# Optimization experiments

Measured on AMD Instinct MI355X. Metric: run time of the kernel, lower is better.

Reference implementation:

```python
import jax, jax.numpy as jnp
import numpy as np

B, IN, HID, OUT = 65536, 128, 256, 8


def setup_inputs() -> dict:
    key = jax.random.key(0)
    ks = jax.random.split(key, 9)
    def lin(kw, fan_in, fan_out):
        # torch nn.Linear default init: U(-1/sqrt(fan_in), 1/sqrt(fan_in))
        bound = 1.0 / np.sqrt(fan_in)
        kw1, kw2 = jax.random.split(kw)
        W = jax.random.uniform(kw1, (fan_out, fan_in), jnp.float32, -bound, bound)
        b = jax.random.uniform(kw2, (fan_out,), jnp.float32, -bound, bound)
        return W, b
    W1, b1 = lin(ks[0], 2 * IN, HID)
    W2, b2 = lin(ks[1], 2 * IN, HID)
    W3, b3 = lin(ks[2], HID + 3 * IN, HID)
    W4, b4 = lin(ks[3], HID, OUT)
    state = jax.random.normal(ks[4], (B, 3, IN), jnp.float32)
    return {"state": state, "W1": W1, "b1": b1, "W2": W2, "b2": b2,
            "W3": W3, "b3": b3, "W4": W4, "b4": b4}


def reference(state, W1, b1, W2, b2, W3, b3, W4, b4):
    # local_inputs = first 3 agents (state already [B,3,IN])
    local = state[:, :3]                              # [B,3,IN]
    agent = jnp.broadcast_to(local[:, :1], (local.shape[0], 2, local.shape[2]))
    neighbors = local[:, 1:3]                          # [B,2,IN]
    agents = jnp.concatenate([agent, neighbors], axis=-1)  # [B,2,2*IN]
    h_ij = jax.nn.relu(jnp.einsum('bnd,hd->bnh', agents, W1) + b1)  # [B,2,HID]
    e_ij = jax.nn.relu(jnp.einsum('bnd,hd->bnh', agents, W2) + b2)  # [B,2,HID]
    a_ij = jax.nn.softmax(e_ij, axis=1)                # softmax over neighbor dim
    h_i = jnp.sum(a_ij * h_ij, axis=1)                 # [B,HID]
    xxx = jnp.concatenate([h_i, local.reshape(local.shape[0], -1)], axis=-1)
    xxx = jax.nn.relu(xxx @ W3.T + b3)                 # [B,HID]
    return jnp.tanh(xxx @ W4.T + b4)                   # [B,OUT]
```

## Files before the change

### kernel.cpp

```cpp
#include <hip/hip_runtime.h>

typedef __bf16 bf16x8 __attribute__((ext_vector_type(8)));
typedef float  f32x4  __attribute__((ext_vector_type(4)));

__device__ __forceinline__ unsigned short f2bf(float f) {
  unsigned int u = __builtin_bit_cast(unsigned int, f);
  u = u + 0x7fffu + ((u >> 16) & 1u);
  return (unsigned short)(u >> 16);
}

#define O_W2 65536
#define O_W3 131072
#define O_W4 294912
#define N_PREP 299008

__global__ void prep_kernel(const float* __restrict__ W1, const float* __restrict__ W2,
                            const float* __restrict__ W3, const float* __restrict__ W4,
                            unsigned short* __restrict__ ws) {
  int id = blockIdx.x * 256 + threadIdx.x;
  if (id < O_W2) {
    ws[id] = f2bf(W1[id]);
  } else if (id < O_W3) {
    ws[id] = f2bf(W2[id - O_W2]);
  } else if (id < O_W4) {
    ws[id] = f2bf(W3[id - O_W3]);
  } else if (id < N_PREP) {
    int t = id - O_W4;
    ws[id] = (t < 2048) ? f2bf(W4[t]) : (unsigned short)0;
  }
}

#define XSTR 648
#define YSTR 264

__global__ __launch_bounds__(512, 2) void actor_kernel(
    const float* __restrict__ state,
    const float* __restrict__ b1, const float* __restrict__ b2,
    const float* __restrict__ b3, const float* __restrict__ b4,
    const unsigned short* __restrict__ wsb,
    float* __restrict__ out)
{
  __shared__ unsigned short xxx[64 * XSTR];
  __shared__ unsigned short ytl[64 * YSTR];

  const int tid  = threadIdx.x;
  const int w    = tid >> 6;
  const int lane = tid & 63;
  const int lr   = lane & 15;
  const int lg   = lane >> 4;
  const long b0  = (long)blockIdx.x * 64;

  {
    const float4* sp = (const float4*)(state + b0 * 384);
    #pragma unroll
    for (int t = 0; t < 12; ++t) {
      int f = tid + t * 512;
      float4 v = sp[f];
      int r   = f / 96;
      int rem = f - r * 96;
      int i   = rem >> 5;
      int k4  = (rem & 31) << 2;
      ushort4 u;
      u.x = f2bf(v.x); u.y = f2bf(v.y); u.z = f2bf(v.z); u.w = f2bf(v.w);
      *(ushort4*)&xxx[r * XSTR + 256 + i * 128 + k4] = u;
    }
  }
  __syncthreads();

  const int n0 = w * 32;

  #pragma unroll
  for (int sc = 0; sc < 2; ++sc) {
    const int ncol = n0 + sc * 16 + lr;
    f32x4 accH[8], accE[8];
    #pragma unroll
    for (int rt = 0; rt < 8; ++rt) {
      accH[rt] = (f32x4){0.f, 0.f, 0.f, 0.f};
      accE[rt] = (f32x4){0.f, 0.f, 0.f, 0.f};
    }
    const unsigned short* w1p = wsb + ncol * 256 + lg * 8;
    const unsigned short* w2p = wsb + O_W2 + ncol * 256 + lg * 8;

    bf16x8 bh = *(const bf16x8*)(w1p);
    bf16x8 be = *(const bf16x8*)(w2p);
    #pragma unroll
    for (int ks = 0; ks < 8; ++ks) {
      bf16x8 bhn, ben;
      if (ks < 7) {
        bhn = *(const bf16x8*)(w1p + (ks + 1) * 32);
        ben = *(const bf16x8*)(w2p + (ks + 1) * 32);
      }
      const int colo = (ks < 4) ? (256 + ks * 32 + lg * 8)
                                : (384 + (ks - 4) * 32 + lg * 8);
      #pragma unroll
      for (int rt = 0; rt < 8; ++rt) {
        const int m = rt * 16 + lr;
        const int addr = (m >> 1) * XSTR + colo + ((ks >= 4) ? ((m & 1) << 7) : 0);
        bf16x8 a = *(const bf16x8*)&xxx[addr];
        accH[rt] = __builtin_amdgcn_mfma_f32_16x16x32_bf16(a, bh, accH[rt], 0, 0, 0);
        accE[rt] = __builtin_amdgcn_mfma_f32_16x16x32_bf16(a, be, accE[rt], 0, 0, 0);
      }
      bh = bhn; be = ben;
    }

    const float b1v = b1[ncol];
    const float b2v = b2[ncol];
    #pragma unroll
    for (int rt = 0; rt < 8; ++rt) {
      const int r0 = rt * 8 + lg * 2;
      #pragma unroll
      for (int pr = 0; pr < 2; ++pr) {
        float h0 = fmaxf(accH[rt][2 * pr + 0] + b1v, 0.f);
        float h1 = fmaxf(accH[rt][2 * pr + 1] + b1v, 0.f);
        float e0 = fmaxf(accE[rt][2 * pr + 0] + b2v, 0.f);
        float e1 = fmaxf(accE[rt][2 * pr + 1] + b2v, 0.f);
        float a0 = 1.0f / (1.0f + __expf(e1 - e0));
        float hi = h1 + a0 * (h0 - h1);
        xxx[(r0 + pr) * XSTR + ncol] = f2bf(hi);
      }
    }
  }
  __syncthreads();

  {
    f32x4 acc3[4][2];
    #pragma unroll
    for (int rt = 0; rt < 4; ++rt) {
      acc3[rt][0] = (f32x4){0.f, 0.f, 0.f, 0.f};
      acc3[rt][1] = (f32x4){0.f, 0.f, 0.f, 0.f};
    }
    const unsigned short* w3pa = wsb + O_W3 + (n0 + lr) * 640 + lg * 8;
    const unsigned short* w3pb = wsb + O_W3 + (n0 + 16 + lr) * 640 + lg * 8;
    bf16x8 ba = *(const bf16x8*)(w3pa);
    bf16x8 bb = *(const bf16x8*)(w3pb);
    for (int ks = 0; ks < 20; ++ks) {
      bf16x8 ban, bbn;
      if (ks < 19) {
        ban = *(const bf16x8*)(w3pa + (ks + 1) * 32);
        bbn = *(const bf16x8*)(w3pb + (ks + 1) * 32);
      }
      #pragma unroll
      for (int rt = 0; rt < 4; ++rt) {
        bf16x8 a = *(const bf16x8*)&xxx[(rt * 16 + lr) * XSTR + ks * 32 + lg * 8];
        acc3[rt][0] = __builtin_amdgcn_mfma_f32_16x16x32_bf16(a, ba, acc3[rt][0], 0, 0, 0);
        acc3[rt][1] = __builtin_amdgcn_mfma_f32_16x16x32_bf16(a, bb, acc3[rt][1], 0, 0, 0);
      }
      ba = ban; bb = bbn;
    }
    const float b3a = b3[n0 + lr];
    const float b3b = b3[n0 + 16 + lr];
    #pragma unroll
    for (int rt = 0; rt < 4; ++rt) {
      #pragma unroll
      for (int reg = 0; reg < 4; ++reg) {
        int row = rt * 16 + lg * 4 + reg;
        float va = fmaxf(acc3[rt][0][reg] + b3a, 0.f);
        float vb = fmaxf(acc3[rt][1][reg] + b3b, 0.f);
        ytl[row * YSTR + n0 + lr]      = f2bf(va);
        ytl[row * YSTR + n0 + 16 + lr] = f2bf(vb);
      }
    }
  }
  __syncthreads();

  if (w < 4) {
    f32x4 acc4 = (f32x4){0.f, 0.f, 0.f, 0.f};
    const unsigned short* w4p = wsb + O_W4 + lr * 256 + lg * 8;
    #pragma unroll
    for (int ks = 0; ks < 8; ++ks) {
      bf16x8 a = *(const bf16x8*)&ytl[(w * 16 + lr) * YSTR + ks * 32 + lg * 8];
      bf16x8 b = *(const bf16x8*)(w4p + ks * 32);
      acc4 = __builtin_amdgcn_mfma_f32_16x16x32_bf16(a, b, acc4, 0, 0, 0);
    }
    if (lr < 8) {
      const float b4v = b4[lr];
      #pragma unroll
      for (int reg = 0; reg < 4; ++reg) {
        long row = b0 + w * 16 + lg * 4 + reg;
        out[row * 8 + lr] = tanhf(acc4[reg] + b4v);
      }
    }
  }
}

extern "C" void kernel_launch(void* const* d_in, const int* in_sizes, int n_in,
                              void* d_out, int out_size, void* d_ws, size_t ws_size,
                              hipStream_t stream) {
  const float* state = (const float*)d_in[0];
  const float* W1 = (const float*)d_in[1];
  const float* b1 = (const float*)d_in[2];
  const float* W2 = (const float*)d_in[3];
  const float* b2 = (const float*)d_in[4];
  const float* W3 = (const float*)d_in[5];
  const float* b3 = (const float*)d_in[6];
  const float* W4 = (const float*)d_in[7];
  const float* b4 = (const float*)d_in[8];

  unsigned short* wsb = (unsigned short*)d_ws;

  prep_kernel<<<(N_PREP + 255) / 256, 256, 0, stream>>>(W1, W2, W3, W4, wsb);
  actor_kernel<<<1024, 512, 0, stream>>>(state, b1, b2, b3, b4, wsb, (float*)d_out);
}
```

Measured before the change: 241.6 us.

## Retile MFMA warps 2D, XOR-swizzle shared memory, reuse one LDS buffer, raise occupancy

Replaces the padded shared-memory strides with an XOR swizzle on a 640-wide row and drops the separate ytl buffer, writing the layer-3 output back into xxx after an extra barrier. This shrinks LDS use so launch bounds can ask for four blocks per CU. Warps are retiled in 2D for layers 1 and 3 so each A fragment feeds four MFMAs, which cuts LDS reads per MFMA. tanhf is also replaced with an exp-based formula. In exchange the kernel carries more accumulators, which raises register pressure against the higher occupancy target.

```diff
diff --git a/kernel.cpp b/kernel.cpp
--- a/kernel.cpp
+++ b/kernel.cpp
@@ -30,18 +30,18 @@
   }
 }
 
-#define XSTR 648
-#define YSTR 264
-
-__global__ __launch_bounds__(512, 2) void actor_kernel(
+#define SX(r, c) ((r) * 640 + ((c) ^ (((r) & 7) << 3)))
+
+#define MFMA __builtin_amdgcn_mfma_f32_16x16x32_bf16
+
+__global__ __launch_bounds__(512, 4) void actor_kernel(
     const float* __restrict__ state,
     const float* __restrict__ b1, const float* __restrict__ b2,
     const float* __restrict__ b3, const float* __restrict__ b4,
     const unsigned short* __restrict__ wsb,
     float* __restrict__ out)
 {
-  __shared__ unsigned short xxx[64 * XSTR];
-  __shared__ unsigned short ytl[64 * YSTR];
+  __shared__ __align__(16) unsigned short xxx[64 * 640];
 
   const int tid  = threadIdx.x;
   const int w    = tid >> 6;
@@ -62,103 +62,131 @@
       int k4  = (rem & 31) << 2;
       ushort4 u;
       u.x = f2bf(v.x); u.y = f2bf(v.y); u.z = f2bf(v.z); u.w = f2bf(v.w);
-      *(ushort4*)&xxx[r * XSTR + 256 + i * 128 + k4] = u;
-    }
-  }
-  __syncthreads();
-
-  const int n0 = w * 32;
-
+      *(ushort4*)&xxx[SX(r, 256 + i * 128 + k4)] = u;
+    }
+  }
+  __syncthreads();
+
+  const int wm = w >> 2;
+  const int wn = w & 3;
   #pragma unroll
   for (int sc = 0; sc < 2; ++sc) {
-    const int ncol = n0 + sc * 16 + lr;
-    f32x4 accH[8], accE[8];
-    #pragma unroll
-    for (int rt = 0; rt < 8; ++rt) {
-      accH[rt] = (f32x4){0.f, 0.f, 0.f, 0.f};
-      accE[rt] = (f32x4){0.f, 0.f, 0.f, 0.f};
-    }
-    const unsigned short* w1p = wsb + ncol * 256 + lg * 8;
-    const unsigned short* w2p = wsb + O_W2 + ncol * 256 + lg * 8;
-
-    bf16x8 bh = *(const bf16x8*)(w1p);
-    bf16x8 be = *(const bf16x8*)(w2p);
+    const int nb = wn * 64 + sc * 32;
+    f32x4 acc[4][4];
+    #pragma unroll
+    for (int rt = 0; rt < 4; ++rt)
+      #pragma unroll
+      for (int c = 0; c < 4; ++c)
+        acc[rt][c] = (f32x4){0.f, 0.f, 0.f, 0.f};
+
+    const unsigned short* w1p = wsb + (nb + lr) * 256 + lg * 8;
+    const unsigned short* w2p = wsb + O_W2 + (nb + lr) * 256 + lg * 8;
+    bf16x8 bh0 = *(const bf16x8*)(w1p);
+    bf16x8 bh1 = *(const bf16x8*)(w1p + 16 * 256);
+    bf16x8 be0 = *(const bf16x8*)(w2p);
+    bf16x8 be1 = *(const bf16x8*)(w2p + 16 * 256);
+    const float bv1a = b1[nb + lr], bv1b = b1[nb + 16 + lr];
+    const float bv2a = b2[nb + lr], bv2b = b2[nb + 16 + lr];
+
     #pragma unroll
     for (int ks = 0; ks < 8; ++ks) {
-      bf16x8 bhn, ben;
+      bf16x8 nh0, nh1, ne0, ne1;
       if (ks < 7) {
-        bhn = *(const bf16x8*)(w1p + (ks + 1) * 32);
-        ben = *(const bf16x8*)(w2p + (ks + 1) * 32);
+        nh0 = *(const bf16x8*)(w1p + (ks + 1) * 32);
+        nh1 = *(const bf16x8*)(w1p + 16 * 256 + (ks + 1) * 32);
+        ne0 = *(const bf16x8*)(w2p + (ks + 1) * 32);
+        ne1 = *(const bf16x8*)(w2p + 16 * 256 + (ks + 1) * 32);
       }
       const int colo = (ks < 4) ? (256 + ks * 32 + lg * 8)
                                 : (384 + (ks - 4) * 32 + lg * 8);
-      #pragma unroll
-      for (int rt = 0; rt < 8; ++rt) {
-        const int m = rt * 16 + lr;
-        const int addr = (m >> 1) * XSTR + colo + ((ks >= 4) ? ((m & 1) << 7) : 0);
-        bf16x8 a = *(const bf16x8*)&xxx[addr];
-        accH[rt] = __builtin_amdgcn_mfma_f32_16x16x32_bf16(a, bh, accH[rt], 0, 0, 0);
-        accE[rt] = __builtin_amdgcn_mfma_f32_16x16x32_bf16(a, be, accE[rt], 0, 0, 0);
-      }
-      bh = bhn; be = ben;
-    }
-
-    const float b1v = b1[ncol];
-    const float b2v = b2[ncol];
-    #pragma unroll
-    for (int rt = 0; rt < 8; ++rt) {
-      const int r0 = rt * 8 + lg * 2;
+      const int po   = (ks >= 4) ? ((lr & 1) << 7) : 0;
+      #pragma unroll
+      for (int rt = 0; rt < 4; ++rt) {
+        const int r = wm * 32 + rt * 8 + (lr >> 1);
+        bf16x8 a = *(const bf16x8*)&xxx[SX(r, colo + po)];
+        acc[rt][0] = MFMA(a, bh0, acc[rt][0], 0, 0, 0);
+        acc[rt][1] = MFMA(a, bh1, acc[rt][1], 0, 0, 0);
+        acc[rt][2] = MFMA(a, be0, acc[rt][2], 0, 0, 0);
+        acc[rt][3] = MFMA(a, be1, acc[rt][3], 0, 0, 0);
+      }
+      if (ks < 7) { bh0 = nh0; bh1 = nh1; be0 = ne0; be1 = ne1; }
+    }
+
+    #pragma unroll
+    for (int rt = 0; rt < 4; ++rt) {
       #pragma unroll
       for (int pr = 0; pr < 2; ++pr) {
-        float h0 = fmaxf(accH[rt][2 * pr + 0] + b1v, 0.f);
-        float h1 = fmaxf(accH[rt][2 * pr + 1] + b1v, 0.f);
-        float e0 = fmaxf(accE[rt][2 * pr + 0] + b2v, 0.f);
-        float e1 = fmaxf(accE[rt][2 * pr + 1] + b2v, 0.f);
-        float a0 = 1.0f / (1.0f + __expf(e1 - e0));
-        float hi = h1 + a0 * (h0 - h1);
-        xxx[(r0 + pr) * XSTR + ncol] = f2bf(hi);
-      }
-    }
-  }
-  __syncthreads();
+        const int r = wm * 32 + rt * 8 + lg * 2 + pr;
+        {
+          float h0 = fmaxf(acc[rt][0][2 * pr + 0] + bv1a, 0.f);
+          float h1 = fmaxf(acc[rt][0][2 * pr + 1] + bv1a, 0.f);
+          float e0 = fmaxf(acc[rt][2][2 * pr + 0] + bv2a, 0.f);
+          float e1 = fmaxf(acc[rt][2][2 * pr + 1] + bv2a, 0.f);
+          float a0 = 1.0f / (1.0f + __expf(e1 - e0));
+          xxx[SX(r, nb + lr)] = f2bf(h1 + a0 * (h0 - h1));
+        }
+        {
+          float h0 = fmaxf(acc[rt][1][2 * pr + 0] + bv1b, 0.f);
+          float h1 = fmaxf(acc[rt][1][2 * pr + 1] + bv1b, 0.f);
+          float e0 = fmaxf(acc[rt][3][2 * pr + 0] + bv2b, 0.f);
+          float e1 = fmaxf(acc[rt][3][2 * pr + 1] + bv2b, 0.f);
+          float a0 = 1.0f / (1.0f + __expf(e1 - e0));
+          xxx[SX(r, nb + 16 + lr)] = f2bf(h1 + a0 * (h0 - h1));
+        }
+      }
+    }
+  }
+  __syncthreads();
+
+  const int wm3 = w & 1;
+  const int wn3 = w >> 1;
+  f32x4 acc3[2][4];
+  #pragma unroll
+  for (int rt = 0; rt < 2; ++rt)
+    #pragma unroll
+    for (int nt = 0; nt < 4; ++nt)
+      acc3[rt][nt] = (f32x4){0.f, 0.f, 0.f, 0.f};
 
   {
-    f32x4 acc3[4][2];
-    #pragma unroll
-    for (int rt = 0; rt < 4; ++rt) {
-      acc3[rt][0] = (f32x4){0.f, 0.f, 0.f, 0.f};
-      acc3[rt][1] = (f32x4){0.f, 0.f, 0.f, 0.f};
-    }
-    const unsigned short* w3pa = wsb + O_W3 + (n0 + lr) * 640 + lg * 8;
-    const unsigned short* w3pb = wsb + O_W3 + (n0 + 16 + lr) * 640 + lg * 8;
-    bf16x8 ba = *(const bf16x8*)(w3pa);
-    bf16x8 bb = *(const bf16x8*)(w3pb);
+    const unsigned short* w3p = wsb + O_W3 + (wn3 * 64 + lr) * 640 + lg * 8;
+    bf16x8 c0 = *(const bf16x8*)(w3p);
+    bf16x8 c1 = *(const bf16x8*)(w3p + 16 * 640);
+    bf16x8 c2 = *(const bf16x8*)(w3p + 32 * 640);
+    bf16x8 c3 = *(const bf16x8*)(w3p + 48 * 640);
     for (int ks = 0; ks < 20; ++ks) {
-      bf16x8 ban, bbn;
+      bf16x8 d0, d1, d2, d3;
       if (ks < 19) {
-        ban = *(const bf16x8*)(w3pa + (ks + 1) * 32);
-        bbn = *(const bf16x8*)(w3pb + (ks + 1) * 32);
-      }
-      #pragma unroll
-      for (int rt = 0; rt < 4; ++rt) {
-        bf16x8 a = *(const bf16x8*)&xxx[(rt * 16 + lr) * XSTR + ks * 32 + lg * 8];
-        acc3[rt][0] = __builtin_amdgcn_mfma_f32_16x16x32_bf16(a, ba, acc3[rt][0], 0, 0, 0);
-        acc3[rt][1] = __builtin_amdgcn_mfma_f32_16x16x32_bf16(a, bb, acc3[rt][1], 0, 0, 0);
-      }
-      ba = ban; bb = bbn;
-    }
-    const float b3a = b3[n0 + lr];
-    const float b3b = b3[n0 + 16 + lr];
-    #pragma unroll
-    for (int rt = 0; rt < 4; ++rt) {
-      #pragma unroll
-      for (int reg = 0; reg < 4; ++reg) {
-        int row = rt * 16 + lg * 4 + reg;
-        float va = fmaxf(acc3[rt][0][reg] + b3a, 0.f);
-        float vb = fmaxf(acc3[rt][1][reg] + b3b, 0.f);
-        ytl[row * YSTR + n0 + lr]      = f2bf(va);
-        ytl[row * YSTR + n0 + 16 + lr] = f2bf(vb);
-      }
+        d0 = *(const bf16x8*)(w3p + (ks + 1) * 32);
+        d1 = *(const bf16x8*)(w3p + 16 * 640 + (ks + 1) * 32);
+        d2 = *(const bf16x8*)(w3p + 32 * 640 + (ks + 1) * 32);
+        d3 = *(const bf16x8*)(w3p + 48 * 640 + (ks + 1) * 32);
+      }
+      #pragma unroll
+      for (int rt = 0; rt < 2; ++rt) {
+        bf16x8 a = *(const bf16x8*)&xxx[SX(wm3 * 32 + rt * 16 + lr, ks * 32 + lg * 8)];
+        acc3[rt][0] = MFMA(a, c0, acc3[rt][0], 0, 0, 0);
+        acc3[rt][1] = MFMA(a, c1, acc3[rt][1], 0, 0, 0);
+        acc3[rt][2] = MFMA(a, c2, acc3[rt][2], 0, 0, 0);
+        acc3[rt][3] = MFMA(a, c3, acc3[rt][3], 0, 0, 0);
+      }
+      if (ks < 19) { c0 = d0; c1 = d1; c2 = d2; c3 = d3; }
+    }
+  }
+  const float bv3_0 = b3[wn3 * 64 + lr];
+  const float bv3_1 = b3[wn3 * 64 + 16 + lr];
+  const float bv3_2 = b3[wn3 * 64 + 32 + lr];
+  const float bv3_3 = b3[wn3 * 64 + 48 + lr];
+  __syncthreads();
+
+  #pragma unroll
+  for (int rt = 0; rt < 2; ++rt) {
+    #pragma unroll
+    for (int reg = 0; reg < 4; ++reg) {
+      const int row = wm3 * 32 + rt * 16 + lg * 4 + reg;
+      xxx[SX(row, wn3 * 64 + lr)]      = f2bf(fmaxf(acc3[rt][0][reg] + bv3_0, 0.f));
+      xxx[SX(row, wn3 * 64 + 16 + lr)] = f2bf(fmaxf(acc3[rt][1][reg] + bv3_1, 0.f));
+      xxx[SX(row, wn3 * 64 + 32 + lr)] = f2bf(fmaxf(acc3[rt][2][reg] + bv3_2, 0.f));
+      xxx[SX(row, wn3 * 64 + 48 + lr)] = f2bf(fmaxf(acc3[rt][3][reg] + bv3_3, 0.f));
     }
   }
   __syncthreads();
@@ -168,16 +196,19 @@
     const unsigned short* w4p = wsb + O_W4 + lr * 256 + lg * 8;
     #pragma unroll
     for (int ks = 0; ks < 8; ++ks) {
-      bf16x8 a = *(const bf16x8*)&ytl[(w * 16 + lr) * YSTR + ks * 32 + lg * 8];
+      bf16x8 a = *(const bf16x8*)&xxx[SX(w * 16 + lr, ks * 32 + lg * 8)];
       bf16x8 b = *(const bf16x8*)(w4p + ks * 32);
-      acc4 = __builtin_amdgcn_mfma_f32_16x16x32_bf16(a, b, acc4, 0, 0, 0);
+      acc4 = MFMA(a, b, acc4, 0, 0, 0);
     }
     if (lr < 8) {
       const float b4v = b4[lr];
       #pragma unroll
       for (int reg = 0; reg < 4; ++reg) {
+        float x = acc4[reg] + b4v;
+        float z = __expf(-2.f * fabsf(x));
+        float t = (1.f - z) / (1.f + z);
         long row = b0 + w * 16 + lg * 4 + reg;
-        out[row * 8 + lr] = tanhf(acc4[reg] + b4v);
+        out[row * 8 + lr] = copysignf(t, x);
       }
     }
   }
```

Result: slower. 286.6 us (+18.6%).

## Swizzle shared tile, merge H/E GEMMs into one MFMA, reuse LDS buffer

Applied to the files above, without the earlier changes.

Replaces padded LDS strides with an XOR-swizzled 640-wide layout and drops the separate ytl buffer, reusing xxx for the layer-3 output after an extra barrier. The first stage now packs W1 and W2 columns into one 16-wide MFMA tile (8 H + 8 E columns) and exchanges E values via shfl_xor, which halves the accumulator count. Weight loads use a 3-deep register ring prefetch, and tanhf is replaced by an exp-based formula. Occupancy hint goes from 2 to 4 blocks per CU, trading fewer registers and less LDS per block for more waves in flight. The cost is an extra barrier and more loop iterations in stage one.

```diff
diff --git a/kernel.cpp b/kernel.cpp
--- a/kernel.cpp
+++ b/kernel.cpp
@@ -30,18 +30,17 @@
   }
 }
 
-#define XSTR 648
-#define YSTR 264
-
-__global__ __launch_bounds__(512, 2) void actor_kernel(
+#define SX(r, c) ((r) * 640 + ((c) ^ (((r) & 7) << 3)))
+#define MFMA __builtin_amdgcn_mfma_f32_16x16x32_bf16
+
+__global__ __launch_bounds__(512, 4) void actor_kernel(
     const float* __restrict__ state,
     const float* __restrict__ b1, const float* __restrict__ b2,
     const float* __restrict__ b3, const float* __restrict__ b4,
     const unsigned short* __restrict__ wsb,
     float* __restrict__ out)
 {
-  __shared__ unsigned short xxx[64 * XSTR];
-  __shared__ unsigned short ytl[64 * YSTR];
+  __shared__ __align__(16) unsigned short xxx[64 * 640];
 
   const int tid  = threadIdx.x;
   const int w    = tid >> 6;
@@ -53,111 +52,110 @@
   {
     const float4* sp = (const float4*)(state + b0 * 384);
     #pragma unroll
-    for (int t = 0; t < 12; ++t) {
-      int f = tid + t * 512;
+    for (int i = 0; i < 12; ++i) {
+      int f = tid + i * 512;
       float4 v = sp[f];
-      int r   = f / 96;
-      int rem = f - r * 96;
-      int i   = rem >> 5;
-      int k4  = (rem & 31) << 2;
+      int r = f / 96, rem = f - r * 96;
       ushort4 u;
       u.x = f2bf(v.x); u.y = f2bf(v.y); u.z = f2bf(v.z); u.w = f2bf(v.w);
-      *(ushort4*)&xxx[r * XSTR + 256 + i * 128 + k4] = u;
+      *(ushort4*)&xxx[SX(r, 256 + rem * 4)] = u;
     }
   }
   __syncthreads();
 
-  const int n0 = w * 32;
-
-  #pragma unroll
-  for (int sc = 0; sc < 2; ++sc) {
-    const int ncol = n0 + sc * 16 + lr;
-    f32x4 accH[8], accE[8];
+  #pragma unroll 1
+  for (int p = 0; p < 4; ++p) {
+    const int cb = w * 32 + p * 8;
+    const unsigned short* wp = (lr < 8)
+        ? (wsb + (cb + lr) * 256 + lg * 8)
+        : (wsb + O_W2 + (cb + (lr - 8)) * 256 + lg * 8);
+    const float bv1 = b1[cb + (lr & 7)];
+    const float bv2 = b2[cb + (lr & 7)];
+
+    bf16x8 ring[4];
+    ring[0] = *(const bf16x8*)(wp);
+    ring[1] = *(const bf16x8*)(wp + 32);
+    ring[2] = *(const bf16x8*)(wp + 64);
+
+    f32x4 acc[8];
+    #pragma unroll
+    for (int rt = 0; rt < 8; ++rt) acc[rt] = (f32x4){0.f, 0.f, 0.f, 0.f};
+
+    #pragma unroll
+    for (int ks = 0; ks < 8; ++ks) {
+      if (ks < 5) ring[(ks + 3) & 3] = *(const bf16x8*)(wp + (ks + 3) * 32);
+      const int colk = (ks < 4) ? (256 + ks * 32 + lg * 8)
+                                : (384 + ((lr & 1) << 7) + (ks - 4) * 32 + lg * 8);
+      #pragma unroll
+      for (int rt = 0; rt < 8; ++rt) {
+        const int r = rt * 8 + (lr >> 1);
+        bf16x8 a = *(const bf16x8*)&xxx[SX(r, colk)];
+        acc[rt] = MFMA(a, ring[ks & 3], acc[rt], 0, 0, 0);
+      }
+    }
+
     #pragma unroll
     for (int rt = 0; rt < 8; ++rt) {
-      accH[rt] = (f32x4){0.f, 0.f, 0.f, 0.f};
-      accE[rt] = (f32x4){0.f, 0.f, 0.f, 0.f};
-    }
-    const unsigned short* w1p = wsb + ncol * 256 + lg * 8;
-    const unsigned short* w2p = wsb + O_W2 + ncol * 256 + lg * 8;
-
-    bf16x8 bh = *(const bf16x8*)(w1p);
-    bf16x8 be = *(const bf16x8*)(w2p);
-    #pragma unroll
-    for (int ks = 0; ks < 8; ++ks) {
-      bf16x8 bhn, ben;
-      if (ks < 7) {
-        bhn = *(const bf16x8*)(w1p + (ks + 1) * 32);
-        ben = *(const bf16x8*)(w2p + (ks + 1) * 32);
-      }
-      const int colo = (ks < 4) ? (256 + ks * 32 + lg * 8)
-                                : (384 + (ks - 4) * 32 + lg * 8);
-      #pragma unroll
-      for (int rt = 0; rt < 8; ++rt) {
-        const int m = rt * 16 + lr;
-        const int addr = (m >> 1) * XSTR + colo + ((ks >= 4) ? ((m & 1) << 7) : 0);
-        bf16x8 a = *(const bf16x8*)&xxx[addr];
-        accH[rt] = __builtin_amdgcn_mfma_f32_16x16x32_bf16(a, bh, accH[rt], 0, 0, 0);
-        accE[rt] = __builtin_amdgcn_mfma_f32_16x16x32_bf16(a, be, accE[rt], 0, 0, 0);
-      }
-      bh = bhn; be = ben;
-    }
-
-    const float b1v = b1[ncol];
-    const float b2v = b2[ncol];
-    #pragma unroll
-    for (int rt = 0; rt < 8; ++rt) {
-      const int r0 = rt * 8 + lg * 2;
-      #pragma unroll
-      for (int pr = 0; pr < 2; ++pr) {
-        float h0 = fmaxf(accH[rt][2 * pr + 0] + b1v, 0.f);
-        float h1 = fmaxf(accH[rt][2 * pr + 1] + b1v, 0.f);
-        float e0 = fmaxf(accE[rt][2 * pr + 0] + b2v, 0.f);
-        float e1 = fmaxf(accE[rt][2 * pr + 1] + b2v, 0.f);
-        float a0 = 1.0f / (1.0f + __expf(e1 - e0));
-        float hi = h1 + a0 * (h0 - h1);
-        xxx[(r0 + pr) * XSTR + ncol] = f2bf(hi);
+      float o0 = __shfl_xor(acc[rt][0], 8);
+      float o1 = __shfl_xor(acc[rt][1], 8);
+      float o2 = __shfl_xor(acc[rt][2], 8);
+      float o3 = __shfl_xor(acc[rt][3], 8);
+      #pragma unroll
+      for (int q = 0; q < 2; ++q) {
+        float h0 = fmaxf(acc[rt][2 * q + 0] + bv1, 0.f);
+        float h1 = fmaxf(acc[rt][2 * q + 1] + bv1, 0.f);
+        float e0 = fmaxf((q ? o2 : o0) + bv2, 0.f);
+        float e1 = fmaxf((q ? o3 : o1) + bv2, 0.f);
+        float a0w = 1.0f / (1.0f + __expf(e1 - e0));
+        float hi = h1 + a0w * (h0 - h1);
+        if (lr < 8) {
+          const int r = rt * 8 + lg * 2 + q;
+          xxx[SX(r, cb + lr)] = f2bf(hi);
+        }
       }
     }
   }
   __syncthreads();
 
   {
+    const int n3 = w * 32;
+    const unsigned short* w3p = wsb + O_W3 + (n3 + lr) * 640 + lg * 8;
+    const float bv3a = b3[n3 + lr];
+    const float bv3b = b3[n3 + 16 + lr];
+
+    bf16x8 ring3[4][2];
+    #pragma unroll
+    for (int k = 0; k < 3; ++k) {
+      ring3[k][0] = *(const bf16x8*)(w3p + k * 32);
+      ring3[k][1] = *(const bf16x8*)(w3p + 16 * 640 + k * 32);
+    }
     f32x4 acc3[4][2];
     #pragma unroll
     for (int rt = 0; rt < 4; ++rt) {
       acc3[rt][0] = (f32x4){0.f, 0.f, 0.f, 0.f};
       acc3[rt][1] = (f32x4){0.f, 0.f, 0.f, 0.f};
     }
-    const unsigned short* w3pa = wsb + O_W3 + (n0 + lr) * 640 + lg * 8;
-    const unsigned short* w3pb = wsb + O_W3 + (n0 + 16 + lr) * 640 + lg * 8;
-    bf16x8 ba = *(const bf16x8*)(w3pa);
-    bf16x8 bb = *(const bf16x8*)(w3pb);
+    #pragma unroll 4
     for (int ks = 0; ks < 20; ++ks) {
-      bf16x8 ban, bbn;
-      if (ks < 19) {
-        ban = *(const bf16x8*)(w3pa + (ks + 1) * 32);
-        bbn = *(const bf16x8*)(w3pb + (ks + 1) * 32);
+      if (ks < 17) {
+        ring3[(ks + 3) & 3][0] = *(const bf16x8*)(w3p + (ks + 3) * 32);
+        ring3[(ks + 3) & 3][1] = *(const bf16x8*)(w3p + 16 * 640 + (ks + 3) * 32);
       }
       #pragma unroll
       for (int rt = 0; rt < 4; ++rt) {
-        bf16x8 a = *(const bf16x8*)&xxx[(rt * 16 + lr) * XSTR + ks * 32 + lg * 8];
-        acc3[rt][0] = __builtin_amdgcn_mfma_f32_16x16x32_bf16(a, ba, acc3[rt][0], 0, 0, 0);
-        acc3[rt][1] = __builtin_amdgcn_mfma_f32_16x16x32_bf16(a, bb, acc3[rt][1], 0, 0, 0);
-      }
-      ba = ban; bb = bbn;
-    }
-    const float b3a = b3[n0 + lr];
-    const float b3b = b3[n0 + 16 + lr];
+        bf16x8 a = *(const bf16x8*)&xxx[SX(rt * 16 + lr, ks * 32 + lg * 8)];
+        acc3[rt][0] = MFMA(a, ring3[ks & 3][0], acc3[rt][0], 0, 0, 0);
+        acc3[rt][1] = MFMA(a, ring3[ks & 3][1], acc3[rt][1], 0, 0, 0);
+      }
+    }
+    __syncthreads();
     #pragma unroll
     for (int rt = 0; rt < 4; ++rt) {
       #pragma unroll
       for (int reg = 0; reg < 4; ++reg) {
-        int row = rt * 16 + lg * 4 + reg;
-        float va = fmaxf(acc3[rt][0][reg] + b3a, 0.f);
-        float vb = fmaxf(acc3[rt][1][reg] + b3b, 0.f);
-        ytl[row * YSTR + n0 + lr]      = f2bf(va);
-        ytl[row * YSTR + n0 + 16 + lr] = f2bf(vb);
+        const int row = rt * 16 + lg * 4 + reg;
+        xxx[SX(row, n3 + lr)]      = f2bf(fmaxf(acc3[rt][0][reg] + bv3a, 0.f));
+        xxx[SX(row, n3 + 16 + lr)] = f2bf(fmaxf(acc3[rt][1][reg] + bv3b, 0.f));
       }
     }
   }
@@ -168,16 +166,19 @@
     const unsigned short* w4p = wsb + O_W4 + lr * 256 + lg * 8;
     #pragma unroll
     for (int ks = 0; ks < 8; ++ks) {
-      bf16x8 a = *(const bf16x8*)&ytl[(w * 16 + lr) * YSTR + ks * 32 + lg * 8];
+      bf16x8 a = *(const bf16x8*)&xxx[SX(w * 16 + lr, ks * 32 + lg * 8)];
       bf16x8 b = *(const bf16x8*)(w4p + ks * 32);
-      acc4 = __builtin_amdgcn_mfma_f32_16x16x32_bf16(a, b, acc4, 0, 0, 0);
+      acc4 = MFMA(a, b, acc4, 0, 0, 0);
     }
     if (lr < 8) {
       const float b4v = b4[lr];
       #pragma unroll
       for (int reg = 0; reg < 4; ++reg) {
+        float x = acc4[reg] + b4v;
+        float z = __expf(-2.f * fabsf(x));
+        float t = (1.f - z) / (1.f + z);
         long row = b0 + w * 16 + lg * 4 + reg;
-        out[row * 8 + lr] = tanhf(acc4[reg] + b4v);
+        out[row * 8 + lr] = copysignf(t, x);
       }
     }
   }
```

Result: no change. 237.3 us (-1.8%).
